# Optimization experiments

Measured on AMD Instinct MI355X. Metric: run time of the kernel, lower is better.

## Reference

```python
import jax, jax.numpy as jnp
import numpy as np

B, S, T = 32, 512, 50          # batch, max seq, topic memory tokens
D, H, F, NL = 512, 8, 2048, 4  # bert-small dims
VB, VOC = 30000, 30522         # bow vocab (VAE), bert vocab


def _ln(x, g, b, eps=1e-12):
    m = x.mean(-1, keepdims=True)
    v = ((x - m) ** 2).mean(-1, keepdims=True)
    return (x - m) * jax.lax.rsqrt(v + eps) * g + b


def setup_inputs() -> dict:
    key = jax.random.key(0)
    ks = iter(jax.random.split(key, 40))
    n = lambda shape, s=0.02: jax.random.normal(next(ks), shape, jnp.float32) * s
    inp = {
        'input_ids': jax.random.randint(next(ks), (B, S), 0, VOC, jnp.int32),
        'seq_lens': jax.random.randint(next(ks), (B,), 1, S + 1, jnp.int32),
        'embed': n((VOC, D)),
        'W_dec': n((T, VB)), 'b_dec': jnp.zeros((VB,), jnp.float32),
        'mem_W1': n((VB, 2 * D)), 'mem_b1': jnp.zeros((2 * D,), jnp.float32),
        'mem_W2': n((2 * D, D)), 'mem_b2': jnp.zeros((D,), jnp.float32),
        'mem_ln_g': jnp.ones((D,), jnp.float32), 'mem_ln_b': jnp.zeros((D,), jnp.float32),
        'Wq': n((NL, D, D)), 'bq': jnp.zeros((NL, D), jnp.float32),
        'Wk': n((NL, D, D)), 'bk': jnp.zeros((NL, D), jnp.float32),
        'Wv': n((NL, D, D)), 'bv': jnp.zeros((NL, D), jnp.float32),
        'Wo': n((NL, D, D)), 'bo': jnp.zeros((NL, D), jnp.float32),
        'ln1_g': jnp.ones((NL, D), jnp.float32), 'ln1_b': jnp.zeros((NL, D), jnp.float32),
        'Wi': n((NL, D, F)), 'bi': jnp.zeros((NL, F), jnp.float32),
        'Wf': n((NL, F, D)), 'bf': jnp.zeros((NL, D), jnp.float32),
        'ln2_g': jnp.ones((NL, D), jnp.float32), 'ln2_b': jnp.zeros((NL, D), jnp.float32),
    }
    return inp


def reference(input_ids, seq_lens, embed, W_dec, b_dec, mem_W1, mem_b1, mem_W2, mem_b2,
              mem_ln_g, mem_ln_b, Wq, bq, Wk, bk, Wv, bv, Wo, bo, ln1_g, ln1_b,
              Wi, bi, Wf, bf, ln2_g, ln2_b):
    # --- topic memory: VAE.decode(eye(T)) == rows of decoder weight ---
    word_dist = jax.nn.softmax(W_dec + b_dec, axis=1)            # [T, VB]
    hmem = jax.nn.relu(word_dist @ mem_W1 + mem_b1)
    topic_memory = _ln(hmem @ mem_W2 + mem_b2, mem_ln_g, mem_ln_b)  # [T, D]

    hidden = embed[input_ids]                                     # [B, S, D]

    # --- vectorized ragged insertion: [real tokens | memory | padding] ---
    lens = jnp.clip(seq_lens, 1, S)[:, None]                      # [B, 1]
    j = jnp.arange(S + T)[None, :]                                # [1, S+T]
    from_mem = (j >= lens) & (j < lens + T)                       # [B, S+T]
    src = jnp.clip(jnp.where(j < lens, j, j - T), 0, S - 1)       # [B, S+T]
    gathered = jnp.take_along_axis(hidden, src[..., None], axis=1)
    mem_idx = jnp.clip(j - lens, 0, T - 1)                        # [B, S+T]
    hidden = jnp.where(from_mem[..., None], topic_memory[mem_idx], gathered)  # [B, S+T, D]
    mask = (j < lens + T).astype(hidden.dtype)                    # [B, S+T]
    bias = (mask - 1.0)[:, None, None, :] * 10000.0               # extended attention mask

    dh = D // H
    scale = 1.0 / np.sqrt(dh)
    for l in range(NL):
        q = (hidden @ Wq[l] + bq[l]).reshape(B, S + T, H, dh)
        k = (hidden @ Wk[l] + bk[l]).reshape(B, S + T, H, dh)
        v = (hidden @ Wv[l] + bv[l]).reshape(B, S + T, H, dh)
        scores = jnp.einsum('bqhd,bkhd->bhqk', q, k) * scale + bias
        attn = jax.nn.softmax(scores, axis=-1)
        ctx = jnp.einsum('bhqk,bkhd->bqhd', attn, v).reshape(B, S + T, D)
        hidden = _ln(hidden + ctx @ Wo[l] + bo[l], ln1_g[l], ln1_b[l])
        ff = jax.nn.gelu(hidden @ Wi[l] + bi[l], approximate=False)
        hidden = _ln(hidden + ff @ Wf[l] + bf[l], ln2_g[l], ln2_b[l])
    return hidden
```

## Files before the change

### kernel.cpp

```cpp
#include <hip/hip_runtime.h>
#include <hip/hip_bf16.h>
#include <math.h>

using bf16 = __hip_bfloat16;
typedef __attribute__((ext_vector_type(4))) float f32x4;
typedef __attribute__((ext_vector_type(8))) short short8;

#define B_N 32
#define S_N 512
#define T_N 50
#define H_N 8
#define NL_N 4
#define VB_N 30000
#define VBP_N 30016
#define ST_N 562
#define STP_N 576
#define NTOK_N (B_N*ST_N)
#define WCH_N 16
#define WCW_N 1875

__device__ __forceinline__ float b2f(bf16 x){ return __bfloat162float(x); }
__device__ __forceinline__ bf16  f2b(float x){ return __float2bfloat16(x); }
__device__ __forceinline__ float ldw(const void* p, long i, int f){
    return f ? ((const float*)p)[i] : __bfloat162float(((const bf16*)p)[i]);
}

__device__ __forceinline__ void load_lds16(const void* g, void* l){
    __builtin_amdgcn_global_load_lds((const __attribute__((address_space(1))) void*)g,
                                     (__attribute__((address_space(3))) void*)l, 16, 0, 0);
}

__device__ __forceinline__ float block_reduce_max(float v, float* red, int t){
    for (int o=32;o>0;o>>=1) v = fmaxf(v, __shfl_down(v,o,64));
    int w=t>>6, lane=t&63;
    if (lane==0) red[w]=v;
    __syncthreads();
    return fmaxf(fmaxf(red[0],red[1]),fmaxf(red[2],red[3]));
}
__device__ __forceinline__ float block_reduce_sum(float v, float* red, int t){
    for (int o=32;o>0;o>>=1) v += __shfl_down(v,o,64);
    int w=t>>6, lane=t&63;
    if (lane==0) red[w]=v;
    __syncthreads();
    return red[0]+red[1]+red[2]+red[3];
}

__global__ __launch_bounds__(256) void detect_k(const unsigned int* __restrict__ w, int* flag)
{
    int t = threadIdx.x;
    float s = 0.f;
    for (int i=t;i<4096;i+=256){ int e = (w[i]>>7)&0xFF; s += fabsf((float)e - 120.f); }
    __shared__ float red[4];
    for (int o=32;o>0;o>>=1) s += __shfl_down(s,o,64);
    int wv=t>>6, lane=t&63;
    if (lane==0) red[wv]=s;
    __syncthreads();
    if (t==0) flag[0] = ((red[0]+red[1]+red[2]+red[3]) * (1.f/4096.f) > 20.f) ? 1 : 0;
}

__global__ void zero_u32_k(unsigned int* p, long n){
    long i = (long)blockIdx.x*256 + threadIdx.x;
    if (i < n) p[i] = 0u;
}

__global__ __launch_bounds__(256) void wd_partmax_k(
    const void* __restrict__ Wd, const void* __restrict__ bd,
    float* __restrict__ pmax, const int* __restrict__ flagp)
{
    const int isf = *flagp;
    int ch = blockIdx.x, r = blockIdx.y, t = threadIdx.x;
    int c0 = ch*WCW_N, c1 = c0 + WCW_N;
    __shared__ float red[4];
    float mx = -1e30f;
    for (int c=c0+t;c<c1;c+=256) mx = fmaxf(mx, ldw(Wd,(long)r*VB_N+c,isf) + ldw(bd,c,isf));
    mx = block_reduce_max(mx, red, t);
    if (t==0) pmax[r*WCH_N + ch] = mx;
}

__global__ __launch_bounds__(256) void wd_partsum_k(
    const void* __restrict__ Wd, const void* __restrict__ bd,
    const float* __restrict__ pmax, float* __restrict__ psum, const int* __restrict__ flagp)
{
    const int isf = *flagp;
    int ch = blockIdx.x, r = blockIdx.y, t = threadIdx.x;
    float mx = -1e30f;
    #pragma unroll
    for (int i=0;i<WCH_N;i++) mx = fmaxf(mx, pmax[r*WCH_N+i]);
    int c0 = ch*WCW_N, c1 = c0 + WCW_N;
    __shared__ float red[4];
    float sm = 0.f;
    for (int c=c0+t;c<c1;c+=256) sm += __expf(ldw(Wd,(long)r*VB_N+c,isf) + ldw(bd,c,isf) - mx);
    sm = block_reduce_sum(sm, red, t);
    if (t==0) psum[r*WCH_N + ch] = sm;
}

__global__ __launch_bounds__(256) void wd_write_k(
    const void* __restrict__ Wd, const void* __restrict__ bd,
    const float* __restrict__ pmax, const float* __restrict__ psum,
    bf16* __restrict__ wdb, const int* __restrict__ flagp)
{
    const int isf = *flagp;
    int ch = blockIdx.x, r = blockIdx.y, t = threadIdx.x;
    float mx = -1e30f, sm = 0.f;
    #pragma unroll
    for (int i=0;i<WCH_N;i++){ mx = fmaxf(mx, pmax[r*WCH_N+i]); sm += psum[r*WCH_N+i]; }
    float inv = 1.f/sm;
    int c0 = ch*WCW_N, c1 = c0 + WCW_N;
    for (int c=c0+t;c<c1;c+=256)
        wdb[(long)r*VBP_N + c] = f2b(__expf(ldw(Wd,(long)r*VB_N+c,isf) + ldw(bd,c,isf) - mx)*inv);
}

__global__ __launch_bounds__(256) void relu_bias_k(
    const float* __restrict__ hmem, const void* __restrict__ b1,
    bf16* __restrict__ hrel, const int* __restrict__ flagp)
{
    const int isf = *flagp;
    int r = blockIdx.x, t = threadIdx.x;
    for (int c=t;c<1024;c+=256){
        float v = (r < T_N) ? fmaxf(hmem[r*1024+c] + ldw(b1,c,isf), 0.f) : 0.f;
        hrel[r*1024+c] = f2b(v);
    }
}

__global__ __launch_bounds__(256) void ln_topic_k(
    const float* __restrict__ fcout,
    const void* __restrict__ lg, const void* __restrict__ lb,
    float* __restrict__ tmf, bf16* __restrict__ tmb, const int* __restrict__ flagp)
{
    const int isf = *flagp;
    int r = blockIdx.x, t = threadIdx.x;
    float a0 = fcout[r*512+t], a1 = fcout[r*512+t+256];
    __shared__ float red[4];
    float mean = block_reduce_sum(a0+a1, red, t) * (1.f/512.f);
    float d0=a0-mean, d1=a1-mean;
    __syncthreads();
    float var = block_reduce_sum(d0*d0+d1*d1, red, t) * (1.f/512.f);
    float rstd = rsqrtf(var + 1e-12f);
    float o0 = d0*rstd*ldw(lg,t,isf) + ldw(lb,t,isf);
    float o1 = d1*rstd*ldw(lg,t+256,isf) + ldw(lb,t+256,isf);
    tmf[r*512+t]=o0; tmf[r*512+t+256]=o1;
    tmb[r*512+t]=f2b(o0); tmb[r*512+t+256]=f2b(o1);
}

__global__ __launch_bounds__(256) void embed_insert_k(
    const int* __restrict__ ids, const int* __restrict__ lens,
    const void* __restrict__ embed, const float* __restrict__ tmf,
    const bf16* __restrict__ tmb, float* __restrict__ hf, bf16* __restrict__ hb,
    const int* __restrict__ flagp)
{
    const int isf = *flagp;
    int j = blockIdx.x, b = blockIdx.y, t = threadIdx.x;
    int L = lens[b]; L = L<1?1:(L>S_N?S_N:L);
    long orow = ((long)b*ST_N + j)*512;
    if (j >= L && j < L + T_N) {
        int m = j - L;
        for (int c=t;c<512;c+=256){ float v = tmf[m*512+c]; hf[orow+c]=v; hb[orow+c]=tmb[m*512+c]; }
    } else {
        int sj = (j < L) ? j : j - T_N;
        int id = ids[b*S_N + sj];
        for (int c=t;c<512;c+=256){ float e = ldw(embed,(long)id*512+c,isf); hf[orow+c]=e; hb[orow+c]=f2b(e); }
    }
}

__global__ __launch_bounds__(256) void transpose_k(
    const void* __restrict__ src, bf16* __restrict__ dst,
    int R, int C, long sstride, long dstride, int Ksrc, const int* __restrict__ flagp)
{
    const int isf = *flagp;
    __shared__ bf16 tile[32][33];
    int n0 = blockIdx.x * 32, k0 = blockIdx.y * 32, z = blockIdx.z;
    int t = threadIdx.x;
    int nl = t & 31, kb = t >> 5;
    #pragma unroll
    for (int i=0;i<4;i++) {
        int k = k0 + kb + i*8; k = k < Ksrc ? k : Ksrc-1;
        tile[kb+i*8][nl] = f2b(ldw(src, z*sstride + (long)k*C + n0+nl, isf));
    }
    __syncthreads();
    int kl = t & 31, nb = t >> 5;
    #pragma unroll
    for (int i=0;i<4;i++) {
        int n = nb + i*8;
        dst[z*dstride + (long)(n0+n)*R + k0+kl] = tile[kl][n];
    }
}

__global__ void concat_bias_k(const void* bq, const void* bk, const void* bv, bf16* out,
                              const int* __restrict__ flagp){
    const int isf = *flagp;
    int i = blockIdx.x*256 + threadIdx.x;
    if (i >= NL_N*1536) return;
    int l = i/1536, n = i%1536;
    float v = (n<512) ? ldw(bq,l*512+n,isf) : (n<1024 ? ldw(bk,l*512+n-512,isf) : ldw(bv,l*512+n-1024,isf));
    out[i] = f2b(v);
}

__global__ __launch_bounds__(256) void transpose_v_k(
    const bf16* __restrict__ qkv, bf16* __restrict__ Vt, const int* __restrict__ slens)
{
    __shared__ bf16 tl[64*33];
    int k0 = blockIdx.x * 32, z = blockIdx.z;
    int b = z >> 3, h = z & 7;
    int L = slens[b]; L = L<1?1:(L>S_N?S_N:L);
    int kmax = ((L + T_N + 63) >> 6) << 6;
    if (k0 >= kmax) return;
    int t = threadIdx.x;
    int n = t & 63, kb = t >> 6;
    #pragma unroll
    for (int i=0;i<8;i++) {
        int kl = kb + 4*i;
        int kg = k0 + kl;
        bf16 v = (kg < ST_N) ? qkv[((long)(b*ST_N + kg))*1536 + 1024 + h*64 + n] : f2b(0.f);
        tl[n*33 + kl] = v;
    }
    __syncthreads();
    int kk = t & 31, nb = t >> 5;
    #pragma unroll
    for (int i=0;i<8;i++) {
        int nn = nb + 8*i;
        Vt[((long)z*64 + nn)*STP_N + k0 + kk] = tl[nn*33 + kk];
    }
}

constexpr int EPI_BF16=0, EPI_F32=1, EPI_GELU=2, EPI_ATOMIC=3, EPI_BF16R=4;

template<int BM, int BN, int MODE>
__global__ __launch_bounds__(256,4) void gemm_k(
    const bf16* __restrict__ Ag, const bf16* __restrict__ Bg, void* __restrict__ Cg,
    const void* __restrict__ bias, long bias_off,
    int M, int N, int K, int lda, int ldb, int ldc, int Nst, int kch,
    const int* __restrict__ flagp)
{
    const int isf = *flagp;
    __shared__ __align__(16) bf16 lA[BM*64];
    __shared__ __align__(16) bf16 lB[BN*64];
    const int tid = threadIdx.x;
    const int tile_m = blockIdx.y * BM;
    const int tile_n = blockIdx.x * BN;

    bf16*  C16 = (bf16*)Cg;
    float* C32 = (float*)Cg;

    constexpr int WM = BM/2, WN = BN/2, MI = WM/16, NI = WN/16;
    const int w = tid>>6, lane = tid&63;
    const int wm = w>>1, wn = w&1;
    const int quad = lane>>4, lrow = lane&15;

    f32x4 zero = {0.f,0.f,0.f,0.f};
    f32x4 acc[MI][NI];
    #pragma unroll
    for (int i=0;i<MI;i++)
        #pragma unroll
        for (int j=0;j<NI;j++) acc[i][j] = zero;

    int ks = 0, ke = K;
    if (kch > 0) { ks = blockIdx.z * kch; ke = ks + kch; if (ke > K) ke = K; }

    for (int k0=ks;k0<ke;k0+=64) {
        __syncthreads();
        #pragma unroll
        for (int r=0;r<BM/32;r++) {
            int e = r*256 + tid;
            int row = e>>3, c8 = (e&7) ^ (row&7);
            int gr = tile_m + row; gr = gr < M ? gr : M-1;
            load_lds16(Ag + (long)gr*lda + k0 + c8*8, &lA[e*8]);
        }
        #pragma unroll
        for (int r=0;r<BN/32;r++) {
            int e = r*256 + tid;
            int row = e>>3, c8 = (e&7) ^ (row&7);
            int gr = tile_n + row; gr = gr < N ? gr : N-1;
            load_lds16(Bg + (long)gr*ldb + k0 + c8*8, &lB[e*8]);
        }
        __syncthreads();
        #pragma unroll
        for (int kc=0;kc<2;kc++){
            short8 afr[MI], bfr[NI];
            #pragma unroll
            for (int i=0;i<MI;i++){
                int row = wm*WM + i*16 + lrow;
                afr[i] = *(const short8*)&lA[row*64 + (((kc*4+quad) ^ (row&7))<<3)];
            }
            #pragma unroll
            for (int j=0;j<NI;j++){
                int row = wn*WN + j*16 + lrow;
                bfr[j] = *(const short8*)&lB[row*64 + (((kc*4+quad) ^ (row&7))<<3)];
            }
            #pragma unroll
            for (int i=0;i<MI;i++)
                #pragma unroll
                for (int j=0;j<NI;j++)
                    acc[i][j] = __builtin_amdgcn_mfma_f32_16x16x32_bf16(afr[i], bfr[j], acc[i][j], 0, 0, 0);
        }
    }

    #pragma unroll
    for (int i=0;i<MI;i++) {
        #pragma unroll
        for (int j=0;j<NI;j++) {
            int col = tile_n + wn*WN + j*16 + lrow;
            int rb  = tile_m + wm*WM + i*16 + quad*4;
            #pragma unroll
            for (int r=0;r<4;r++) {
                int row = rb + r;
                if (row >= M || col >= Nst) continue;
                float v = acc[i][j][r];
                if constexpr (MODE == EPI_BF16) {
                    C16[(long)row*ldc + col] = f2b(v + b2f(((const bf16*)bias)[bias_off + col]));
                } else if constexpr (MODE == EPI_F32) {
                    C32[(long)row*ldc + col] = v + ldw(bias, bias_off + col, isf);
                } else if constexpr (MODE == EPI_GELU) {
                    float x = v + ldw(bias, bias_off + col, isf);
                    C16[(long)row*ldc + col] = f2b(0.5f*x*(1.f + erff(x*0.70710678118654752f)));
                } else if constexpr (MODE == EPI_BF16R) {
                    C16[(long)row*ldc + col] = f2b(v + ldw(bias, bias_off + col, isf));
                } else {
                    atomicAdd(&C32[(long)row*ldc + col], v);
                }
            }
        }
    }
}

__global__ __launch_bounds__(256,2) void flash_k(
    const bf16* __restrict__ qkv, const bf16* __restrict__ Vt,
    bf16* __restrict__ ctx, const int* __restrict__ slens)
{
    __shared__ __align__(16) bf16 lQ[128*64];
    __shared__ __align__(16) bf16 lK[64*64];
    __shared__ __align__(16) bf16 lV[64*64];
    __shared__ __align__(16) bf16 lP[128*64];
    const int z = blockIdx.z, b = z>>3, h = z&7;
    const int qt = blockIdx.x;
    const int tid = threadIdx.x;
    const int w = tid>>6, lane = tid&63;
    const int quad = lane>>4, l15 = lane&15;
    int L = slens[b]; L = L<1?1:(L>S_N?S_N:L);
    const int lenT = L + T_N;
    const int nkt = (lenT + 63) >> 6;

    #pragma unroll
    for (int rr=0;rr<4;rr++){
        int ci = rr*256 + tid;
        int row = ci>>3, c8 = (ci&7) ^ (row&7);
        int gr = qt*128 + row; gr = gr < ST_N ? gr : ST_N-1;
        load_lds16(qkv + ((long)(b*ST_N+gr))*1536 + h*64 + c8*8, &lQ[ci*8]);
    }

    f32x4 zerov = {0.f,0.f,0.f,0.f};
    f32x4 O[2][4];
    float m_i[2][4], l_i[2][4];
    #pragma unroll
    for (int i=0;i<2;i++){
        #pragma unroll
        for (int j=0;j<4;j++) O[i][j] = zerov;
        #pragma unroll
        for (int r=0;r<4;r++){ m_i[i][r]=-1e30f; l_i[i][r]=0.f; }
    }

    for (int kt=0; kt<nkt; kt++){
        __syncthreads();
        #pragma unroll
        for (int rr=0;rr<2;rr++){
            int ci = rr*256+tid;
            int row = ci>>3, c8 = (ci&7) ^ (row&7);
            int kr = kt*64+row; kr = kr < ST_N ? kr : ST_N-1;
            load_lds16(qkv + ((long)(b*ST_N+kr))*1536 + 512 + h*64 + c8*8, &lK[ci*8]);
        }
        #pragma unroll
        for (int rr=0;rr<2;rr++){
            int ci = rr*256+tid;
            int n = ci>>3, c8 = (ci&7) ^ (n&7);
            load_lds16(Vt + ((long)z*64+n)*STP_N + kt*64 + c8*8, &lV[ci*8]);
        }
        __syncthreads();

        f32x4 S[2][4];
        #pragma unroll
        for (int i=0;i<2;i++)
            #pragma unroll
            for (int j=0;j<4;j++) S[i][j] = zerov;
        #pragma unroll
        for (int kc=0;kc<2;kc++){
            short8 aQ[2], bK[4];
            #pragma unroll
            for (int i=0;i<2;i++){
                int row = w*32+i*16+l15;
                aQ[i] = *(const short8*)&lQ[row*64 + (((kc*4+quad) ^ (row&7))<<3)];
            }
            #pragma unroll
            for (int j=0;j<4;j++){
                int row = j*16+l15;
                bK[j] = *(const short8*)&lK[row*64 + (((kc*4+quad) ^ (row&7))<<3)];
            }
            #pragma unroll
            for (int i=0;i<2;i++)
                #pragma unroll
                for (int j=0;j<4;j++)
                    S[i][j] = __builtin_amdgcn_mfma_f32_16x16x32_bf16(aQ[i], bK[j], S[i][j], 0,0,0);
        }

        #pragma unroll
        for (int i=0;i<2;i++){
            #pragma unroll
            for (int r=0;r<4;r++){
                float mx = -1e30f;
                #pragma unroll
                for (int j=0;j<4;j++){
                    int col = kt*64 + j*16 + l15;
                    float s = S[i][j][r]*0.125f + (col < lenT ? 0.f : -10000.f);
                    S[i][j][r] = s;
                    mx = fmaxf(mx, s);
                }
                #pragma unroll
                for (int o=1;o<16;o<<=1) mx = fmaxf(mx, __shfl_xor(mx, o, 64));
                float mn = fmaxf(m_i[i][r], mx);
                float alpha = __expf(m_i[i][r] - mn);
                m_i[i][r] = mn;
                float sm = 0.f;
                #pragma unroll
                for (int j=0;j<4;j++){
                    float pv = __expf(S[i][j][r] - mn);
                    S[i][j][r] = pv;
                    sm += pv;
                }
                #pragma unroll
                for (int o=1;o<16;o<<=1) sm += __shfl_xor(sm, o, 64);
                l_i[i][r] = l_i[i][r]*alpha + sm;
                #pragma unroll
                for (int j=0;j<4;j++) O[i][j][r] *= alpha;
            }
        }

        #pragma unroll
        for (int i=0;i<2;i++)
            #pragma unroll
            for (int j=0;j<4;j++)
                #pragma unroll
                for (int r=0;r<4;r++){
                    int row = w*32 + i*16 + quad*4 + r;
                    int col = j*16 + l15;
                    lP[row*64 + (((col>>3) ^ (row&7))<<3) + (col&7)] = f2b(S[i][j][r]);
                }
        __syncthreads();

        #pragma unroll
        for (int kc=0;kc<2;kc++){
            short8 aP[2], bV[4];
            #pragma unroll
            for (int i=0;i<2;i++){
                int row = w*32+i*16+l15;
                aP[i] = *(const short8*)&lP[row*64 + (((kc*4+quad) ^ (row&7))<<3)];
            }
            #pragma unroll
            for (int j=0;j<4;j++){
                int row = j*16+l15;
                bV[j] = *(const short8*)&lV[row*64 + (((kc*4+quad) ^ (row&7))<<3)];
            }
            #pragma unroll
            for (int i=0;i<2;i++)
                #pragma unroll
                for (int j=0;j<4;j++)
                    O[i][j] = __builtin_amdgcn_mfma_f32_16x16x32_bf16(aP[i], bV[j], O[i][j], 0,0,0);
        }
    }

    #pragma unroll
    for (int i=0;i<2;i++)
        #pragma unroll
        for (int j=0;j<4;j++)
            #pragma unroll
            for (int r=0;r<4;r++){
                int row = qt*128 + w*32 + i*16 + quad*4 + r;
                if (row < ST_N)
                    ctx[((long)(b*ST_N+row))*512 + h*64 + j*16 + l15] = f2b(O[i][j][r] / l_i[i][r]);
            }
}

__global__ __launch_bounds__(256) void ln_residual_k(
    const bf16* __restrict__ tmp, float* __restrict__ hf, bf16* __restrict__ hb,
    const void* __restrict__ g, const void* __restrict__ bb, long goff,
    void* __restrict__ outp, int is_final, const int* __restrict__ flagp)
{
    const int isf = *flagp;
    const int of32 = is_final && isf;
    long base = (long)blockIdx.x * 512;
    int t = threadIdx.x;
    float v0 = hf[base+t]     + b2f(tmp[base+t]);
    float v1 = hf[base+t+256] + b2f(tmp[base+t+256]);
    __shared__ float red[4];
    float mean = block_reduce_sum(v0+v1, red, t) * (1.f/512.f);
    float d0=v0-mean, d1=v1-mean;
    __syncthreads();
    float var = block_reduce_sum(d0*d0+d1*d1, red, t) * (1.f/512.f);
    float rstd = rsqrtf(var + 1e-12f);
    float o0 = d0*rstd*ldw(g,goff+t,isf) + ldw(bb,goff+t,isf);
    float o1 = d1*rstd*ldw(g,goff+t+256,isf) + ldw(bb,goff+t+256,isf);
    hf[base+t]=o0; hf[base+t+256]=o1;
    hb[base+t]=f2b(o0); hb[base+t+256]=f2b(o1);
    if (of32) {
        ((float*)outp)[base+t]=o0; ((float*)outp)[base+t+256]=o1;
    } else {
        ((bf16*)outp)[base+t]=f2b(o0); ((bf16*)outp)[base+t+256]=f2b(o1);
    }
}

extern "C" void kernel_launch(void* const* d_in, const int* in_sizes, int n_in,
                              void* d_out, int out_size, void* d_ws, size_t ws_size,
                              hipStream_t stream)
{
    (void)in_sizes; (void)n_in; (void)out_size; (void)ws_size;
    const int*  ids   = (const int*) d_in[0];
    const int*  slens = (const int*) d_in[1];
    const void* embed = d_in[2];
    const void* Wdec  = d_in[3];
    const void* bdec  = d_in[4];
    const void* mW1   = d_in[5];
    const void* mb1   = d_in[6];
    const void* mW2   = d_in[7];
    const void* mb2   = d_in[8];
    const void* mlg   = d_in[9];
    const void* mlb   = d_in[10];
    const void* Wq    = d_in[11];
    const void* bq    = d_in[12];
    const void* Wk    = d_in[13];
    const void* bk    = d_in[14];
    const void* Wv    = d_in[15];
    const void* bv    = d_in[16];
    const void* Wo    = d_in[17];
    const void* bo    = d_in[18];
    const void* l1g   = d_in[19];
    const void* l1b   = d_in[20];
    const void* Wi    = d_in[21];
    const void* bi    = d_in[22];
    const void* Wf    = d_in[23];
    const void* bfv   = d_in[24];
    const void* l2g   = d_in[25];
    const void* l2b   = d_in[26];

    char* p = (char*)d_ws;
    auto alloc = [&](size_t bytes)->void* {
        void* r = (void*)p; p += (bytes + 255) & ~(size_t)255; return r; };
    int*   flag  = (int*)  alloc(256);
    float* pmax  = (float*)alloc((size_t)T_N*WCH_N*4);
    float* psum  = (float*)alloc((size_t)T_N*WCH_N*4);
    float* tmf   = (float*)alloc((size_t)T_N*512*4);
    bf16*  tmb   = (bf16*) alloc((size_t)T_N*512*2);
    float* hmem  = (float*)alloc((size_t)64*1024*4);
    bf16*  hrel  = (bf16*) alloc((size_t)64*1024*2);
    float* fcout = (float*)alloc((size_t)64*512*4);
    float* hidf  = (float*)alloc((size_t)NTOK_N*512*4);
    bf16*  hidb  = (bf16*) alloc((size_t)NTOK_N*512*2);
    bf16*  qkvt  = (bf16*) alloc((size_t)NL_N*1536*512*2);
    bf16*  wot   = (bf16*) alloc((size_t)NL_N*512*512*2);
    bf16*  wit   = (bf16*) alloc((size_t)NL_N*2048*512*2);
    bf16*  wft   = (bf16*) alloc((size_t)NL_N*512*2048*2);
    bf16*  bqkv  = (bf16*) alloc((size_t)NL_N*1536*2);
    char*  R1    = (char*) alloc((size_t)NTOK_N*2048*2);
    bf16*  wdb   = (bf16*)R1;
    bf16*  W1t   = (bf16*)(R1 + (size_t)64*VBP_N*2);
    bf16*  W2t   = (bf16*)(R1 + (size_t)64*VBP_N*2 + (size_t)1024*VBP_N*2);
    bf16*  qkv   = (bf16*)R1;
    bf16*  ffb   = (bf16*)R1;
    bf16*  ctx   = (bf16*) alloc((size_t)NTOK_N*512*2);
    char*  RU2   = (char*) alloc((size_t)NTOK_N*512*4);
    bf16*  Vt    = (bf16*)RU2;
    bf16*  tmp16 = (bf16*)RU2;

    detect_k<<<1,256,0,stream>>>((const unsigned int*)embed, flag);

    zero_u32_k<<<((64L*VBP_N/2)+255)/256,256,0,stream>>>((unsigned int*)wdb, 64L*VBP_N/2);
    zero_u32_k<<<((64L*1024)+255)/256,256,0,stream>>>((unsigned int*)hmem, 64L*1024);
    wd_partmax_k<<<dim3(WCH_N,T_N),256,0,stream>>>(Wdec,bdec,pmax,flag);
    wd_partsum_k<<<dim3(WCH_N,T_N),256,0,stream>>>(Wdec,bdec,pmax,psum,flag);
    wd_write_k  <<<dim3(WCH_N,T_N),256,0,stream>>>(Wdec,bdec,pmax,psum,wdb,flag);
    transpose_k<<<dim3(32,VBP_N/32,1),256,0,stream>>>(mW1, W1t, VBP_N, 1024, 0L, 0L, VB_N, flag);
    transpose_k<<<dim3(16,32,1),256,0,stream>>>(mW2, W2t, 1024, 512, 0L, 0L, 1024, flag);
    gemm_k<64,128,EPI_ATOMIC><<<dim3(8,1,32),256,0,stream>>>(
        wdb, W1t, hmem, nullptr, 0,
        64, 1024, VBP_N, VBP_N, VBP_N, 1024, 1024, 960, flag);
    relu_bias_k<<<64,256,0,stream>>>(hmem, mb1, hrel, flag);
    gemm_k<64,128,EPI_F32><<<dim3(4,1,1),256,0,stream>>>(
        hrel, W2t, fcout, mb2, 0,
        64, 512, 1024, 1024, 1024, 512, 512, 0, flag);
    ln_topic_k<<<T_N,256,0,stream>>>(fcout, mlg, mlb, tmf, tmb, flag);
    embed_insert_k<<<dim3(ST_N,B_N),256,0,stream>>>(ids, slens, embed, tmf, tmb, hidf, hidb, flag);

    transpose_k<<<dim3(16,16,NL_N),256,0,stream>>>(Wq, qkvt,          512, 512, 262144L, 786432L, 512, flag);
    transpose_k<<<dim3(16,16,NL_N),256,0,stream>>>(Wk, qkvt+262144,   512, 512, 262144L, 786432L, 512, flag);
    transpose_k<<<dim3(16,16,NL_N),256,0,stream>>>(Wv, qkvt+524288,   512, 512, 262144L, 786432L, 512, flag);
    transpose_k<<<dim3(16,16,NL_N),256,0,stream>>>(Wo, wot,           512, 512, 262144L, 262144L, 512, flag);
    transpose_k<<<dim3(64,16,NL_N),256,0,stream>>>(Wi, wit,           512, 2048, 1048576L, 1048576L, 512, flag);
    transpose_k<<<dim3(16,64,NL_N),256,0,stream>>>(Wf, wft,           2048, 512, 1048576L, 1048576L, 2048, flag);
    concat_bias_k<<<(NL_N*1536+255)/256,256,0,stream>>>(bq,bk,bv,bqkv,flag);

    for (int l=0;l<NL_N;l++) {
        gemm_k<128,128,EPI_BF16><<<dim3(12,141,1),256,0,stream>>>(
            hidb, qkvt + (size_t)l*786432, qkv, bqkv, (long)l*1536,
            NTOK_N, 1536, 512, 512, 512, 1536, 1536, 0, flag);
        transpose_v_k<<<dim3(18,1,256),256,0,stream>>>(qkv, Vt, slens);
        flash_k<<<dim3(5,1,256),256,0,stream>>>(qkv, Vt, ctx, slens);
        gemm_k<128,128,EPI_BF16R><<<dim3(4,141,1),256,0,stream>>>(
            ctx, wot + (size_t)l*262144, tmp16, bo, (long)l*512,
            NTOK_N, 512, 512, 512, 512, 512, 512, 0, flag);
        ln_residual_k<<<NTOK_N,256,0,stream>>>(tmp16, hidf, hidb, l1g, l1b, (long)l*512,
                                               hidb, 0, flag);
        gemm_k<128,128,EPI_GELU><<<dim3(16,141,1),256,0,stream>>>(
            hidb, wit + (size_t)l*1048576, ffb, bi, (long)l*2048,
            NTOK_N, 2048, 512, 512, 512, 2048, 2048, 0, flag);
        gemm_k<128,128,EPI_BF16R><<<dim3(4,141,1),256,0,stream>>>(
            ffb, wft + (size_t)l*1048576, tmp16, bfv, (long)l*512,
            NTOK_N, 512, 2048, 2048, 2048, 512, 512, 0, flag);
        ln_residual_k<<<NTOK_N,256,0,stream>>>(tmp16, hidf, hidb, l2g, l2b, (long)l*512,
                                               (l == NL_N-1) ? d_out : (void*)hidb,
                                               (l == NL_N-1) ? 1 : 0, flag);
    }
}
```

Measured before the change: 1.805 ms.

## Double-buffer LDS tiles in GEMM and flash attention to overlap loads

The GEMM kernel now uses two LDS buffers with a K-step of 32 instead of one buffer with a K-step of 64. The next tile is issued right after a single barrier per iteration, so it loads while the current tile feeds the MFMAs. The flash attention kernel likewise double-buffers K and V, prefetching the next K tile before QK^T and the next V tile before PV. This aims to hide global-to-LDS latency and cut one barrier per iteration, at the cost of more LDS in flash, twice as many GEMM iterations, and reliance on the loads completing before the next barrier.

```diff
diff --git a/kernel.cpp b/kernel.cpp
--- a/kernel.cpp
+++ b/kernel.cpp
@@ -232,8 +232,8 @@
     const int* __restrict__ flagp)
 {
     const int isf = *flagp;
-    __shared__ __align__(16) bf16 lA[BM*64];
-    __shared__ __align__(16) bf16 lB[BN*64];
+    __shared__ __align__(16) bf16 lA[2][BM*32];
+    __shared__ __align__(16) bf16 lB[2][BN*32];
     const int tid = threadIdx.x;
     const int tile_m = blockIdx.y * BM;
     const int tile_n = blockIdx.x * BN;
@@ -256,42 +256,45 @@
     int ks = 0, ke = K;
     if (kch > 0) { ks = blockIdx.z * kch; ke = ks + kch; if (ke > K) ke = K; }
 
-    for (int k0=ks;k0<ke;k0+=64) {
+    auto stage = [&](int buf, int k0){
+        #pragma unroll
+        for (int r=0;r<BM/64;r++) {
+            int e = r*256 + tid;
+            int row = e>>2, c4 = (e&3) ^ ((row>>1)&3);
+            int gr = tile_m + row; gr = gr < M ? gr : M-1;
+            load_lds16(Ag + (long)gr*lda + k0 + c4*8, &lA[buf][e*8]);
+        }
+        #pragma unroll
+        for (int r=0;r<BN/64;r++) {
+            int e = r*256 + tid;
+            int row = e>>2, c4 = (e&3) ^ ((row>>1)&3);
+            int gr = tile_n + row; gr = gr < N ? gr : N-1;
+            load_lds16(Bg + (long)gr*ldb + k0 + c4*8, &lB[buf][e*8]);
+        }
+    };
+
+    stage(0, ks);
+    int cur = 0;
+    for (int k0=ks;k0<ke;k0+=32) {
         __syncthreads();
-        #pragma unroll
-        for (int r=0;r<BM/32;r++) {
-            int e = r*256 + tid;
-            int row = e>>3, c8 = (e&7) ^ (row&7);
-            int gr = tile_m + row; gr = gr < M ? gr : M-1;
-            load_lds16(Ag + (long)gr*lda + k0 + c8*8, &lA[e*8]);
-        }
-        #pragma unroll
-        for (int r=0;r<BN/32;r++) {
-            int e = r*256 + tid;
-            int row = e>>3, c8 = (e&7) ^ (row&7);
-            int gr = tile_n + row; gr = gr < N ? gr : N-1;
-            load_lds16(Bg + (long)gr*ldb + k0 + c8*8, &lB[e*8]);
-        }
-        __syncthreads();
-        #pragma unroll
-        for (int kc=0;kc<2;kc++){
-            short8 afr[MI], bfr[NI];
-            #pragma unroll
-            for (int i=0;i<MI;i++){
-                int row = wm*WM + i*16 + lrow;
-                afr[i] = *(const short8*)&lA[row*64 + (((kc*4+quad) ^ (row&7))<<3)];
-            }
-            #pragma unroll
-            for (int j=0;j<NI;j++){
-                int row = wn*WN + j*16 + lrow;
-                bfr[j] = *(const short8*)&lB[row*64 + (((kc*4+quad) ^ (row&7))<<3)];
-            }
-            #pragma unroll
-            for (int i=0;i<MI;i++)
-                #pragma unroll
-                for (int j=0;j<NI;j++)
-                    acc[i][j] = __builtin_amdgcn_mfma_f32_16x16x32_bf16(afr[i], bfr[j], acc[i][j], 0, 0, 0);
-        }
+        if (k0+32 < ke) stage(cur^1, k0+32);
+        short8 afr[MI], bfr[NI];
+        #pragma unroll
+        for (int i=0;i<MI;i++){
+            int row = wm*WM + i*16 + lrow;
+            afr[i] = *(const short8*)&lA[cur][row*32 + ((quad ^ ((row>>1)&3))<<3)];
+        }
+        #pragma unroll
+        for (int j=0;j<NI;j++){
+            int row = wn*WN + j*16 + lrow;
+            bfr[j] = *(const short8*)&lB[cur][row*32 + ((quad ^ ((row>>1)&3))<<3)];
+        }
+        #pragma unroll
+        for (int i=0;i<MI;i++)
+            #pragma unroll
+            for (int j=0;j<NI;j++)
+                acc[i][j] = __builtin_amdgcn_mfma_f32_16x16x32_bf16(afr[i], bfr[j], acc[i][j], 0, 0, 0);
+        cur ^= 1;
     }
 
     #pragma unroll
@@ -327,8 +330,8 @@
     bf16* __restrict__ ctx, const int* __restrict__ slens)
 {
     __shared__ __align__(16) bf16 lQ[128*64];
-    __shared__ __align__(16) bf16 lK[64*64];
-    __shared__ __align__(16) bf16 lV[64*64];
+    __shared__ __align__(16) bf16 lK[2][64*64];
+    __shared__ __align__(16) bf16 lV[2][64*64];
     __shared__ __align__(16) bf16 lP[128*64];
     const int z = blockIdx.z, b = z>>3, h = z&7;
     const int qt = blockIdx.x;
@@ -347,33 +350,42 @@
         load_lds16(qkv + ((long)(b*ST_N+gr))*1536 + h*64 + c8*8, &lQ[ci*8]);
     }
 
-    f32x4 zerov = {0.f,0.f,0.f,0.f};
-    f32x4 O[2][4];
-    float m_i[2][4], l_i[2][4];
-    #pragma unroll
-    for (int i=0;i<2;i++){
-        #pragma unroll
-        for (int j=0;j<4;j++) O[i][j] = zerov;
-        #pragma unroll
-        for (int r=0;r<4;r++){ m_i[i][r]=-1e30f; l_i[i][r]=0.f; }
-    }
-
-    for (int kt=0; kt<nkt; kt++){
-        __syncthreads();
+    auto stage_K = [&](int buf, int kt){
         #pragma unroll
         for (int rr=0;rr<2;rr++){
             int ci = rr*256+tid;
             int row = ci>>3, c8 = (ci&7) ^ (row&7);
             int kr = kt*64+row; kr = kr < ST_N ? kr : ST_N-1;
-            load_lds16(qkv + ((long)(b*ST_N+kr))*1536 + 512 + h*64 + c8*8, &lK[ci*8]);
-        }
+            load_lds16(qkv + ((long)(b*ST_N+kr))*1536 + 512 + h*64 + c8*8, &lK[buf][ci*8]);
+        }
+    };
+    auto stage_V = [&](int buf, int kt){
         #pragma unroll
         for (int rr=0;rr<2;rr++){
             int ci = rr*256+tid;
             int n = ci>>3, c8 = (ci&7) ^ (n&7);
-            load_lds16(Vt + ((long)z*64+n)*STP_N + kt*64 + c8*8, &lV[ci*8]);
-        }
+            load_lds16(Vt + ((long)z*64+n)*STP_N + kt*64 + c8*8, &lV[buf][ci*8]);
+        }
+    };
+
+    stage_K(0, 0);
+    stage_V(0, 0);
+
+    f32x4 zerov = {0.f,0.f,0.f,0.f};
+    f32x4 O[2][4];
+    float m_i[2][4], l_i[2][4];
+    #pragma unroll
+    for (int i=0;i<2;i++){
+        #pragma unroll
+        for (int j=0;j<4;j++) O[i][j] = zerov;
+        #pragma unroll
+        for (int r=0;r<4;r++){ m_i[i][r]=-1e30f; l_i[i][r]=0.f; }
+    }
+
+    for (int kt=0; kt<nkt; kt++){
+        const int cur = kt & 1;
         __syncthreads();
+        if (kt+1 < nkt) stage_K(cur^1, kt+1);
 
         f32x4 S[2][4];
         #pragma unroll
@@ -391,7 +403,7 @@
             #pragma unroll
             for (int j=0;j<4;j++){
                 int row = j*16+l15;
-                bK[j] = *(const short8*)&lK[row*64 + (((kc*4+quad) ^ (row&7))<<3)];
+                bK[j] = *(const short8*)&lK[cur][row*64 + (((kc*4+quad) ^ (row&7))<<3)];
             }
             #pragma unroll
             for (int i=0;i<2;i++)
@@ -443,6 +455,7 @@
                     lP[row*64 + (((col>>3) ^ (row&7))<<3) + (col&7)] = f2b(S[i][j][r]);
                 }
         __syncthreads();
+        if (kt+1 < nkt) stage_V(cur^1, kt+1);
 
         #pragma unroll
         for (int kc=0;kc<2;kc++){
@@ -455,7 +468,7 @@
             #pragma unroll
             for (int j=0;j<4;j++){
                 int row = j*16+l15;
-                bV[j] = *(const short8*)&lV[row*64 + (((kc*4+quad) ^ (row&7))<<3)];
+                bV[j] = *(const short8*)&lV[cur][row*64 + (((kc*4+quad) ^ (row&7))<<3)];
             }
             #pragma unroll
             for (int i=0;i<2;i++)
```

Result: slower. 1.910 ms (+5.8%).

## Double-buffer K/V tiles in flash attention and add XCD-aware block swizzle

Applied to the files above, without the earlier changes.

The attention kernel now keeps two LDS buffers for K and V and issues the loads for the next key tile while the current tile is being computed. This hides global-to-LDS latency behind the MFMA and softmax work. Separately, both the GEMM and flash kernels remap the flat block index so that neighbouring tiles land on the same XCD, aiming for better L2 reuse. The cost is doubled K/V LDS use in the flash kernel, which could limit occupancy, plus some index arithmetic.

```diff
diff --git a/kernel.cpp b/kernel.cpp
--- a/kernel.cpp
+++ b/kernel.cpp
@@ -30,6 +30,12 @@
                                      (__attribute__((address_space(3))) void*)l, 16, 0, 0);
 }
 
+__device__ __forceinline__ int xcd_swizzle(int flat, int nwg){
+    int xcd = flat & 7, rest = flat >> 3;
+    int q = nwg >> 3, r = nwg & 7;
+    return (xcd < r ? xcd*(q+1) : r*(q+1) + (xcd-r)*q) + rest;
+}
+
 __device__ __forceinline__ float block_reduce_max(float v, float* red, int t){
     for (int o=32;o>0;o>>=1) v = fmaxf(v, __shfl_down(v,o,64));
     int w=t>>6, lane=t&63;
@@ -235,8 +241,11 @@
     __shared__ __align__(16) bf16 lA[BM*64];
     __shared__ __align__(16) bf16 lB[BN*64];
     const int tid = threadIdx.x;
-    const int tile_m = blockIdx.y * BM;
-    const int tile_n = blockIdx.x * BN;
+    const int nwg = gridDim.x * gridDim.y;
+    const int flat = blockIdx.y * gridDim.x + blockIdx.x;
+    const int swz = xcd_swizzle(flat, nwg);
+    const int tile_m = (swz / gridDim.x) * BM;
+    const int tile_n = (swz % gridDim.x) * BN;
 
     bf16*  C16 = (bf16*)Cg;
     float* C32 = (float*)Cg;
@@ -327,11 +336,14 @@
     bf16* __restrict__ ctx, const int* __restrict__ slens)
 {
     __shared__ __align__(16) bf16 lQ[128*64];
-    __shared__ __align__(16) bf16 lK[64*64];
-    __shared__ __align__(16) bf16 lV[64*64];
+    __shared__ __align__(16) bf16 lK[2][64*64];
+    __shared__ __align__(16) bf16 lV[2][64*64];
     __shared__ __align__(16) bf16 lP[128*64];
-    const int z = blockIdx.z, b = z>>3, h = z&7;
-    const int qt = blockIdx.x;
+    const int nwg = gridDim.x * gridDim.z;
+    const int flat = blockIdx.z * gridDim.x + blockIdx.x;
+    const int swz = xcd_swizzle(flat, nwg);
+    const int z = swz / gridDim.x, b = z>>3, h = z&7;
+    const int qt = swz % gridDim.x;
     const int tid = threadIdx.x;
     const int w = tid>>6, lane = tid&63;
     const int quad = lane>>4, l15 = lane&15;
@@ -347,33 +359,42 @@
         load_lds16(qkv + ((long)(b*ST_N+gr))*1536 + h*64 + c8*8, &lQ[ci*8]);
     }
 
-    f32x4 zerov = {0.f,0.f,0.f,0.f};
-    f32x4 O[2][4];
-    float m_i[2][4], l_i[2][4];
-    #pragma unroll
-    for (int i=0;i<2;i++){
-        #pragma unroll
-        for (int j=0;j<4;j++) O[i][j] = zerov;
-        #pragma unroll
-        for (int r=0;r<4;r++){ m_i[i][r]=-1e30f; l_i[i][r]=0.f; }
-    }
-
-    for (int kt=0; kt<nkt; kt++){
-        __syncthreads();
+    auto stage_K = [&](int buf, int kt){
         #pragma unroll
         for (int rr=0;rr<2;rr++){
             int ci = rr*256+tid;
             int row = ci>>3, c8 = (ci&7) ^ (row&7);
             int kr = kt*64+row; kr = kr < ST_N ? kr : ST_N-1;
-            load_lds16(qkv + ((long)(b*ST_N+kr))*1536 + 512 + h*64 + c8*8, &lK[ci*8]);
-        }
+            load_lds16(qkv + ((long)(b*ST_N+kr))*1536 + 512 + h*64 + c8*8, &lK[buf][ci*8]);
+        }
+    };
+    auto stage_V = [&](int buf, int kt){
         #pragma unroll
         for (int rr=0;rr<2;rr++){
             int ci = rr*256+tid;
             int n = ci>>3, c8 = (ci&7) ^ (n&7);
-            load_lds16(Vt + ((long)z*64+n)*STP_N + kt*64 + c8*8, &lV[ci*8]);
-        }
+            load_lds16(Vt + ((long)z*64+n)*STP_N + kt*64 + c8*8, &lV[buf][ci*8]);
+        }
+    };
+
+    stage_K(0, 0);
+    stage_V(0, 0);
+
+    f32x4 zerov = {0.f,0.f,0.f,0.f};
+    f32x4 O[2][4];
+    float m_i[2][4], l_i[2][4];
+    #pragma unroll
+    for (int i=0;i<2;i++){
+        #pragma unroll
+        for (int j=0;j<4;j++) O[i][j] = zerov;
+        #pragma unroll
+        for (int r=0;r<4;r++){ m_i[i][r]=-1e30f; l_i[i][r]=0.f; }
+    }
+
+    for (int kt=0; kt<nkt; kt++){
+        const int cur = kt & 1;
         __syncthreads();
+        if (kt+1 < nkt) stage_K(cur^1, kt+1);
 
         f32x4 S[2][4];
         #pragma unroll
@@ -391,7 +412,7 @@
             #pragma unroll
             for (int j=0;j<4;j++){
                 int row = j*16+l15;
-                bK[j] = *(const short8*)&lK[row*64 + (((kc*4+quad) ^ (row&7))<<3)];
+                bK[j] = *(const short8*)&lK[cur][row*64 + (((kc*4+quad) ^ (row&7))<<3)];
             }
             #pragma unroll
             for (int i=0;i<2;i++)
@@ -443,6 +464,7 @@
                     lP[row*64 + (((col>>3) ^ (row&7))<<3) + (col&7)] = f2b(S[i][j][r]);
                 }
         __syncthreads();
+        if (kt+1 < nkt) stage_V(cur^1, kt+1);
 
         #pragma unroll
         for (int kc=0;kc<2;kc++){
@@ -455,7 +477,7 @@
             #pragma unroll
             for (int j=0;j<4;j++){
                 int row = j*16+l15;
-                bV[j] = *(const short8*)&lV[row*64 + (((kc*4+quad) ^ (row&7))<<3)];
+                bV[j] = *(const short8*)&lV[cur][row*64 + (((kc*4+quad) ^ (row&7))<<3)];
             }
             #pragma unroll
             for (int i=0;i<2;i++)
```

Result: faster. 1.702 ms (-5.7%).
